# Optimization experiments

Hardware: AMD Instinct MI355X
Metric: run time of the kernel (lower is better)

The kernel has to match this reference:

```python
import jax, jax.numpy as jnp
import numpy as np

B, S, D, H, NUM_REL = 8, 1024, 1024, 16, 512
HD = D // H  # head size = 64


def setup_inputs() -> dict:
    key = jax.random.key(0)
    ks = jax.random.split(key, 12)
    sc = 0.02  # weight init scale for numerical stability
    inp = {
        "query": jax.random.normal(ks[0], (B, S, D), jnp.float32),
        "key": jax.random.normal(ks[1], (B, S, D), jnp.float32),
        "value": jax.random.normal(ks[2], (B, S, D), jnp.float32),
        "Wq": jax.random.normal(ks[3], (D, D), jnp.float32) * sc,
        "bq": jnp.zeros((D,), jnp.float32),
        "Wk": jax.random.normal(ks[4], (D, D), jnp.float32) * sc,
        "bk": jnp.zeros((D,), jnp.float32),
        "Wv": jax.random.normal(ks[5], (D, D), jnp.float32) * sc,
        "bv": jnp.zeros((D,), jnp.float32),
        "Wo": jax.random.normal(ks[6], (D, D), jnp.float32) * sc,
        "bo": jnp.zeros((D,), jnp.float32),
        "pos_table": jax.random.normal(ks[7], (NUM_REL, HD), jnp.float32) * sc,
        # True = masked position (causal: cannot attend to future)
        "mask": jnp.broadcast_to(jnp.triu(jnp.ones((S, S), bool), k=1), (B, S, S)),
    }
    return inp


def reference(query, key, value, Wq, bq, Wk, bk, Wv, bv, Wo, bo, pos_table, mask):
    Bq, Sq, Dm = query.shape
    hd = Dm // H

    def proj(x, W, b):
        # nn.Linear: x @ W.T + b, then split heads -> [B, H, S, hd]
        return (x @ W.T + b).reshape(Bq, Sq, H, hd).transpose(0, 2, 1, 3)

    q = proj(query, Wq, bq)
    k = proj(key, Wk, bk)
    v = proj(value, Wv, bv)

    scores = jnp.einsum("bhid,bhjd->bhij", q, k)

    # relative-position bias: idxs[i,j] = clip(i - j, 0, NUM_REL-1)
    t = jnp.arange(Sq)
    idxs = jnp.clip(t[:, None] - t[None, :], 0, pos_table.shape[0] - 1)
    pos = pos_table[idxs]  # [S, S, hd]
    scores = scores + jnp.einsum("bhid,ijd->bhij", q, pos)

    scores = scores / np.sqrt(hd).astype(np.float32)
    scores = jnp.where(mask[:, None, :, :], jnp.float32(-1e9), scores)
    prob = jax.nn.softmax(scores, axis=-1)  # dropout p=0.0 -> identity

    out = jnp.einsum("bhij,bhjd->bhid", prob, v)
    out = out.transpose(0, 2, 1, 3).reshape(Bq, Sq, Dm)
    return out @ Wo.T + bo
```

## Files before the change

### kernel.cpp

```cpp
#include <hip/hip_runtime.h>
#include <stdint.h>

#define DEV __device__ __forceinline__

typedef unsigned short u16;
typedef __bf16 bf16x8 __attribute__((ext_vector_type(8)));
typedef float  f32x4  __attribute__((ext_vector_type(4)));
typedef unsigned short u16x8 __attribute__((ext_vector_type(8)));
typedef unsigned short u16x4 __attribute__((ext_vector_type(4)));
typedef float  fvec4  __attribute__((ext_vector_type(4)));

constexpr int Sz   = 1024;
constexpr int Dm   = 1024;
constexpr int HDm  = 64;
constexpr int NREL = 512;
constexpr int Mrows = 8192;
constexpr int KV   = 32;

DEV u16 f2bf(float f) { return __builtin_bit_cast(u16, (__bf16)f); }
DEV float bf2f(u16 h) { return __builtin_bit_cast(float, (uint32_t)h << 16); }
DEV f32x4 mfma16(bf16x8 a, bf16x8 b, f32x4 c) {
  return __builtin_amdgcn_mfma_f32_16x16x32_bf16(a, b, c, 0, 0, 0);
}
DEV float ex2(float x) {
  float r;
  asm("v_exp_f32 %0, %1" : "=v"(r) : "v"(x));
  return r;
}

DEV u16x4 tr0(const u16* p) {
  u16x4 d;
  asm volatile("ds_read_b64_tr_b16 %0, %1"
               : "=v"(d)
               : "v"((const __attribute__((address_space(3))) u16*)p));
  return d;
}
DEV u16x4 tr512(const u16* p) {
  u16x4 d;
  asm volatile("ds_read_b64_tr_b16 %0, %1 offset:512"
               : "=v"(d)
               : "v"((const __attribute__((address_space(3))) u16*)p));
  return d;
}
DEV bf16x8 mk8(u16x4 a, u16x4 b) {
  u16x8 r;
  r[0] = a[0]; r[1] = a[1]; r[2] = a[2]; r[3] = a[3];
  r[4] = b[0]; r[5] = b[1]; r[6] = b[2]; r[7] = b[3];
  return __builtin_bit_cast(bf16x8, r);
}
DEV void gload(const u16* src, u16* dst) {
  __builtin_amdgcn_global_load_lds(
      (const __attribute__((address_space(1))) void*)src,
      (__attribute__((address_space(3))) void*)dst, 16, 0, 0);
}

__global__ __launch_bounds__(256) void cvtw_kernel(const float* __restrict__ w0,
                                                   const float* __restrict__ w1,
                                                   const float* __restrict__ w2,
                                                   const float* __restrict__ w3,
                                                   const float* __restrict__ ps,
                                                   u16* __restrict__ o0,
                                                   u16* __restrict__ o1,
                                                   u16* __restrict__ o2,
                                                   u16* __restrict__ o3,
                                                   u16* __restrict__ op) {
  const int bid = blockIdx.x;
  const float* in;
  u16* out;
  int local;
  if (bid < 4096) {
    const int s = bid >> 10;
    in = s == 0 ? w0 : s == 1 ? w1 : s == 2 ? w2 : w3;
    out = s == 0 ? o0 : s == 1 ? o1 : s == 2 ? o2 : o3;
    local = bid & 1023;
  } else {
    in = ps; out = op; local = bid - 4096;
  }
  size_t i = (size_t)local * 256 + threadIdx.x;
  fvec4 v = *(const fvec4*)(in + i * 4);
  u16x4 o;
  o[0] = f2bf(v[0]); o[1] = f2bf(v[1]); o[2] = f2bf(v[2]); o[3] = f2bf(v[3]);
  *(u16x4*)(out + i * 4) = o;
}

template<bool OUT_BF16>
DEV void gemm_epilogue(const float* bias, void* Cout, int m0, int n0,
                       int wr, int wc, int lr, int lg, f32x4 acc[4][4]) {
  #pragma unroll
  for (int m = 0; m < 4; ++m) {
    const int grow = m0 + wr + m * 16 + lr;
    #pragma unroll
    for (int n = 0; n < 4; ++n) {
      const int gcol = n0 + wc + n * 16 + lg * 4;
      fvec4 bb = *(const fvec4*)&bias[gcol];
      if (OUT_BF16) {
        u16x4 w;
        #pragma unroll
        for (int r = 0; r < 4; ++r) w[r] = f2bf(acc[m][n][r] + bb[r]);
        *(u16x4*)&((u16*)Cout)[(size_t)grow * Dm + gcol] = w;
      } else {
        fvec4 w;
        #pragma unroll
        for (int r = 0; r < 4; ++r) w[r] = acc[m][n][r] + bb[r];
        *(fvec4*)&((float*)Cout)[(size_t)grow * Dm + gcol] = w;
      }
    }
  }
}

DEV void gemm_compute(const u16* Ab, const u16* Bb, int wr, int wc,
                      int lr, int lg, f32x4 acc[4][4]) {
  #pragma unroll
  for (int kk = 0; kk < 2; ++kk) {
    bf16x8 af[4], bf_[4];
    #pragma unroll
    for (int m = 0; m < 4; ++m)
      af[m] = *(const bf16x8*)&Ab[(wr + m * 16 + lr) * 64 + (((kk * 4 + lg) ^ (lr & 7)) * 8)];
    #pragma unroll
    for (int n = 0; n < 4; ++n)
      bf_[n] = *(const bf16x8*)&Bb[(wc + n * 16 + lr) * 64 + (((kk * 4 + lg) ^ (lr & 7)) * 8)];
    __builtin_amdgcn_s_setprio(1);
    #pragma unroll
    for (int m = 0; m < 4; ++m)
      #pragma unroll
      for (int n = 0; n < 4; ++n)
        acc[m][n] = mfma16(bf_[n], af[m], acc[m][n]);
    __builtin_amdgcn_s_setprio(0);
  }
}

template<bool OUT_BF16>
DEV void gemm_body16(const u16* __restrict__ A, const u16* __restrict__ Bw,
                     const float* __restrict__ bias, void* __restrict__ Cout,
                     int m0, int n0, u16* As, u16* Bs) {
  const int tid = threadIdx.x;
  const int wave = tid >> 6, lane = tid & 63;
  const int lr = lane & 15, lg = lane >> 4;
  const int wr = (wave >> 1) * 64, wc = (wave & 1) * 64;

  auto issue = [&](int t) {
    const int k0 = t * 64;
    u16* Ad = As + (t & 1) * (128 * 64);
    u16* Bd = Bs + (t & 1) * (128 * 64);
    #pragma unroll
    for (int it = 0; it < 4; ++it) {
      int chunk = it * 256 + tid;
      int row = chunk >> 3, c16 = chunk & 7;
      gload(Bw + (size_t)(n0 + row) * Dm + k0 + ((c16 ^ (row & 7)) * 8),
            Bd + (it * 256 + wave * 64) * 8);
      gload(A + (size_t)(m0 + row) * Dm + k0 + ((c16 ^ (row & 7)) * 8),
            Ad + (it * 256 + wave * 64) * 8);
    }
  };

  issue(0);
  f32x4 acc[4][4] = {};
  for (int t = 0; t < 16; ++t) {
    if (t < 15) {
      issue(t + 1);
      asm volatile("s_waitcnt vmcnt(8)" ::: "memory");
    } else {
      asm volatile("s_waitcnt vmcnt(0)" ::: "memory");
    }
    __builtin_amdgcn_s_barrier();
    gemm_compute(As + (t & 1) * (128 * 64), Bs + (t & 1) * (128 * 64),
                 wr, wc, lr, lg, acc);
    __builtin_amdgcn_s_barrier();
  }
  gemm_epilogue<OUT_BF16>(bias, Cout, m0, n0, wr, wc, lr, lg, acc);
}

template<bool OUT_BF16>
DEV void gemm_body32(const float* __restrict__ A, const u16* __restrict__ Bw,
                     const float* __restrict__ bias, void* __restrict__ Cout,
                     int m0, int n0, u16* As, u16* Bs) {
  const int tid = threadIdx.x;
  const int wave = tid >> 6, lane = tid & 63;
  const int lr = lane & 15, lg = lane >> 4;
  const int wr = (wave >> 1) * 64, wc = (wave & 1) * 64;

  fvec4 ar[4][2];
  auto loadA = [&](int t) {
    const int k0 = t * 64;
    #pragma unroll
    for (int it = 0; it < 4; ++it) {
      int chunk = it * 256 + tid;
      int rw = chunk >> 3, cc = chunk & 7;
      const float* src = A + (size_t)(m0 + rw) * Dm + k0 + cc * 8;
      ar[it][0] = *(const fvec4*)src;
      ar[it][1] = *(const fvec4*)(src + 4);
    }
  };
  auto issueB = [&](int t) {
    const int k0 = t * 64;
    u16* Bd = Bs + (t & 1) * (128 * 64);
    #pragma unroll
    for (int it = 0; it < 4; ++it) {
      int chunk = it * 256 + tid;
      int rw = chunk >> 3, cc = chunk & 7;
      gload(Bw + (size_t)(n0 + rw) * Dm + k0 + ((cc ^ (rw & 7)) * 8),
            Bd + (it * 256 + wave * 64) * 8);
    }
  };

  loadA(0);
  __builtin_amdgcn_sched_barrier(0);
  issueB(0);
  __builtin_amdgcn_sched_barrier(0);

  f32x4 acc[4][4] = {};
  for (int t = 0; t < 16; ++t) {
    asm volatile("s_waitcnt vmcnt(4)" ::: "memory");
    __builtin_amdgcn_sched_barrier(0);
    u16* Ad = As + (t & 1) * (128 * 64);
    #pragma unroll
    for (int it = 0; it < 4; ++it) {
      int chunk = it * 256 + tid;
      int rw = chunk >> 3, cc = chunk & 7;
      u16x8 v;
      #pragma unroll
      for (int e = 0; e < 4; ++e) { v[e] = f2bf(ar[it][0][e]); v[e + 4] = f2bf(ar[it][1][e]); }
      *(u16x8*)&Ad[rw * 64 + ((cc ^ (rw & 7)) * 8)] = v;
    }
    __builtin_amdgcn_sched_barrier(0);
    if (t < 15) {
      loadA(t + 1);
      __builtin_amdgcn_sched_barrier(0);
      issueB(t + 1);
      __builtin_amdgcn_sched_barrier(0);
      asm volatile("s_waitcnt vmcnt(12)" ::: "memory");
    } else {
      asm volatile("s_waitcnt vmcnt(0)" ::: "memory");
    }
    asm volatile("s_waitcnt lgkmcnt(0)" ::: "memory");
    __builtin_amdgcn_s_barrier();
    gemm_compute(Ad, Bs + (t & 1) * (128 * 64), wr, wc, lr, lg, acc);
    __builtin_amdgcn_s_barrier();
  }
  gemm_epilogue<OUT_BF16>(bias, Cout, m0, n0, wr, wc, lr, lg, acc);
}

template<bool OUT_BF16>
__global__ __launch_bounds__(256) void gemm1_kernel(const u16* __restrict__ A,
                                                    const u16* __restrict__ Bw,
                                                    const float* __restrict__ bias,
                                                    void* __restrict__ Cout) {
  __shared__ u16 As[2 * 128 * 64];
  __shared__ u16 Bs[2 * 128 * 64];
  const int r = blockIdx.x;
  const int xcd = r & 7, loc = r >> 3;
  const int m0 = (xcd * 8 + (loc & 7)) * 128;
  const int n0 = (loc >> 3) * 128;
  gemm_body16<OUT_BF16>(A, Bw, bias, Cout, m0, n0, As, Bs);
}

__global__ __launch_bounds__(256) void gemm3_kernel(
    const float* __restrict__ Xq, const float* __restrict__ Xk, const float* __restrict__ Xv,
    const u16* __restrict__ Wq, const u16* __restrict__ Wk, const u16* __restrict__ Wv,
    const float* __restrict__ bq, const float* __restrict__ bk, const float* __restrict__ bv,
    u16* __restrict__ Cq, u16* __restrict__ Ck, u16* __restrict__ Cv) {
  __shared__ u16 As[2 * 128 * 64];
  __shared__ u16 Bs[2 * 128 * 64];
  const int flat = blockIdx.x;
  const int seg = flat >> 9;
  const int r = flat & 511;
  const int xcd = r & 7, loc = r >> 3;
  const int m0 = (xcd * 8 + (loc & 7)) * 128;
  const int n0 = (loc >> 3) * 128;
  const float* A = seg == 0 ? Xq : seg == 1 ? Xk : Xv;
  const u16* Bw = seg == 0 ? Wq : seg == 1 ? Wk : Wv;
  const float* bias = seg == 0 ? bq : seg == 1 ? bk : bv;
  u16* C = seg == 0 ? Cq : seg == 1 ? Ck : Cv;
  gemm_body32<true>(A, Bw, bias, C, m0, n0, As, Bs);
}

__global__ __launch_bounds__(256, 4) void attn_kernel(const u16* __restrict__ Q,
                                                      const u16* __restrict__ Kb,
                                                      const u16* __restrict__ Vb,
                                                      const u16* __restrict__ posB,
                                                      u16* __restrict__ O) {
  __shared__ u16 Ks[2][KV * 64];
  __shared__ u16 Vs[2][KV * 64];
  __shared__ u16 ring[128 * 64];
  __shared__ u16 SH[4][16 * 40];

  const int tid = threadIdx.x;
  const int wave = tid >> 6, lane = tid & 63;
  const int lr = lane & 15, lg = lane >> 4;
  const int bid = blockIdx.x;
  const int xcd = bid & 7;
  const int idx = bid >> 3;
  const int bhl = idx & 15;
  const int pp_ = idx >> 4;
  const int bh  = xcd * 16 + bhl;
  const int b = bh >> 4, h = bh & 15;

  u16* SHW = SH[wave];
  const size_t rowbase = (size_t)(b * Sz) * Dm + h * HDm;

  const int krow = tid >> 3, kc = tid & 7;
  const int vj = ((tid >> 5) << 2) | ((tid >> 1) & 3);
  const int vd = ((tid >> 3) & 3) * 16 + (tid & 1) * 8;
  const int rrow = tid >> 3, rcol = tid & 7;

  auto issueKV = [&](int t) {
    const int j0 = t * KV;
    const int bsel = t & 1;
    gload(Kb + rowbase + (size_t)(j0 + krow) * Dm + ((kc ^ (krow & 7)) * 8),
          &Ks[bsel][wave * 512]);
    gload(Vb + rowbase + (size_t)(j0 + vj) * Dm + vd, &Vs[bsel][wave * 512]);
  };
  auto stageRing = [&](int cb) {
    const int rel = cb + rrow;
    const int slot = rel & 127;
    const int cl = rel < 0 ? 0 : (rel > NREL - 1 ? NREL - 1 : rel);
    gload(posB + cl * 64 + ((rcol ^ (slot & 7)) * 8),
          &ring[((cb & 127) + wave * 8) * 64]);
  };

  constexpr float SC = 0.125f * 1.44269504f;

  for (int job = 0; job < 2; ++job) {
    const int qi = job ? pp_ : 15 - pp_;
    const int qb = qi * 64;
    const int wq = qb + wave * 16;
    const int nt = 2 * qi + 2;
    const int qg = wq + lr;

    const u16* qptr = Q + rowbase + (size_t)(wq + lr) * Dm;
    bf16x8 qf[2];
    qf[0] = *(const bf16x8*)(qptr + lg * 8);
    qf[1] = *(const bf16x8*)(qptr + 32 + lg * 8);

    float b511;
    {
      const u16* pp = posB + (NREL - 1) * HDm;
      bf16x8 pa0 = *(const bf16x8*)(pp + lg * 8);
      bf16x8 pa1 = *(const bf16x8*)(pp + 32 + lg * 8);
      f32x4 a = {};
      a = mfma16(pa0, qf[0], a);
      a = mfma16(pa1, qf[1], a);
      b511 = a[0];
    }

    stageRing(qb + 32);
    stageRing(qb);
    stageRing(qb - 32);
    issueKV(0);

    f32x4 oacc[4] = {};
    float m_i = -1e30f, l_i = 0.f;

    for (int t = 0; t < nt; ++t) {
      const int j0 = t * KV;
      const int bsel = t & 1;
      const bool active = (j0 <= wq + 15);
      const bool clamp = (wq - j0 - 31) >= NREL - 1;
      const int wb = wq - j0 - 31;

      if (t + 1 < nt) {
        stageRing(qb - 32 * (t + 1) - 32);
        issueKV(t + 1);
        asm volatile("s_waitcnt vmcnt(3)" ::: "memory");
      } else {
        asm volatile("s_waitcnt vmcnt(0)" ::: "memory");
      }
      __builtin_amdgcn_s_barrier();

      if (active) {
        if (!clamp) {
          #pragma unroll
          for (int wg = 0; wg < 3; ++wg) {
            const int rrel = wb + wg * 16 + lr;
            const int slot = rrel & 127;
            const u16* rp = &ring[slot * 64];
            f32x4 a = {};
            a = mfma16(qf[0], *(const bf16x8*)&rp[((0 + lg) ^ (slot & 7)) * 8], a);
            a = mfma16(qf[1], *(const bf16x8*)&rp[((4 + lg) ^ (slot & 7)) * 8], a);
            #pragma unroll
            for (int r = 0; r < 4; ++r) {
              const int q = lg * 4 + r;
              const int col = q - (wg * 16 + lr) + 31;
              if (col >= 0 && col < 32)
                SHW[q * 40 + col] = f2bf(a[r]);
            }
          }
        }

        __builtin_amdgcn_s_setprio(1);
        f32x4 s0 = {}, s1 = {};
        const u16* KT = &Ks[bsel][0];
        s0 = mfma16(*(const bf16x8*)&KT[(0 + lr) * 64 + (((0 + lg) ^ (lr & 7)) * 8)], qf[0], s0);
        s0 = mfma16(*(const bf16x8*)&KT[(0 + lr) * 64 + (((4 + lg) ^ (lr & 7)) * 8)], qf[1], s0);
        s1 = mfma16(*(const bf16x8*)&KT[(16 + lr) * 64 + (((0 + lg) ^ (lr & 7)) * 8)], qf[0], s1);
        s1 = mfma16(*(const bf16x8*)&KT[(16 + lr) * 64 + (((4 + lg) ^ (lr & 7)) * 8)], qf[1], s1);
        __builtin_amdgcn_s_setprio(0);

        float p0[4], p1[4];
        float tmax = -3e38f;
        if (clamp) {
          #pragma unroll
          for (int r = 0; r < 4; ++r) {
            p0[r] = (s0[r] + b511) * SC; tmax = fmaxf(tmax, p0[r]);
            p1[r] = (s1[r] + b511) * SC; tmax = fmaxf(tmax, p1[r]);
          }
        } else {
          u16x4 bv0 = *(const u16x4*)&SHW[lr * 40 + lg * 4];
          u16x4 bv1 = *(const u16x4*)&SHW[lr * 40 + 16 + lg * 4];
          #pragma unroll
          for (int r = 0; r < 4; ++r) {
            float v0 = (s0[r] + bf2f(bv0[r])) * SC;
            if (j0 + lg * 4 + r > qg) v0 = -1e9f;
            p0[r] = v0; tmax = fmaxf(tmax, v0);
            float v1 = (s1[r] + bf2f(bv1[r])) * SC;
            if (j0 + 16 + lg * 4 + r > qg) v1 = -1e9f;
            p1[r] = v1; tmax = fmaxf(tmax, v1);
          }
        }
        tmax = fmaxf(tmax, __shfl_xor(tmax, 16));
        tmax = fmaxf(tmax, __shfl_xor(tmax, 32));

        if (!__all(tmax <= m_i + 11.5f)) {
          float mn = fmaxf(m_i, tmax);
          float sc = ex2(m_i - mn);
          m_i = mn; l_i *= sc;
          #pragma unroll
          for (int dg = 0; dg < 4; ++dg) oacc[dg] *= sc;
        }

        float lsum = 0.f;
        #pragma unroll
        for (int r = 0; r < 4; ++r) {
          p0[r] = ex2(p0[r] - m_i); lsum += p0[r];
          p1[r] = ex2(p1[r] - m_i); lsum += p1[r];
        }
        lsum += __shfl_xor(lsum, 16);
        lsum += __shfl_xor(lsum, 32);
        l_i += lsum;

        u16x4 pk0, pk1;
        #pragma unroll
        for (int r = 0; r < 4; ++r) { pk0[r] = f2bf(p0[r]); pk1[r] = f2bf(p1[r]); }
        *(u16x4*)&SHW[lr * 40 + lg * 4] = pk0;
        *(u16x4*)&SHW[lr * 40 + 16 + lg * 4] = pk1;

        bf16x8 pB = *(const bf16x8*)&SHW[lr * 40 + lg * 8];

        u16x4 va[4][2];
        #pragma unroll
        for (int dg = 0; dg < 4; ++dg) {
          const u16* base = &Vs[bsel][(2 * lg) * 256 + dg * 64 + lr * 4];
          va[dg][0] = tr0(base);
          va[dg][1] = tr512(base);
        }
        asm volatile("s_waitcnt lgkmcnt(0)" ::: "memory");
        __builtin_amdgcn_sched_barrier(0);
        __builtin_amdgcn_s_setprio(1);
        #pragma unroll
        for (int dg = 0; dg < 4; ++dg)
          oacc[dg] = mfma16(mk8(va[dg][0], va[dg][1]), pB, oacc[dg]);
        __builtin_amdgcn_s_setprio(0);
      }
      __builtin_amdgcn_s_barrier();
    }

    const float inv = 1.0f / l_i;
    const size_t obase = rowbase + (size_t)qg * Dm;
    #pragma unroll
    for (int dg = 0; dg < 4; ++dg) {
      u16x4 w;
      #pragma unroll
      for (int r = 0; r < 4; ++r) w[r] = f2bf(oacc[dg][r] * inv);
      *(u16x4*)&O[obase + dg * 16 + lg * 4] = w;
    }
  }
}

extern "C" void kernel_launch(void* const* d_in, const int* in_sizes, int n_in,
                              void* d_out, int out_size, void* d_ws, size_t ws_size,
                              hipStream_t stream) {
  const float* query = (const float*)d_in[0];
  const float* key   = (const float*)d_in[1];
  const float* value = (const float*)d_in[2];
  const float* Wq    = (const float*)d_in[3];
  const float* bq    = (const float*)d_in[4];
  const float* Wk    = (const float*)d_in[5];
  const float* bk    = (const float*)d_in[6];
  const float* Wv    = (const float*)d_in[7];
  const float* bv    = (const float*)d_in[8];
  const float* Wo    = (const float*)d_in[9];
  const float* bo    = (const float*)d_in[10];
  const float* pos   = (const float*)d_in[11];

  char* ws = (char*)d_ws;
  u16* WqB  = (u16*)(ws);
  u16* WkB  = (u16*)(ws + (2ull << 20));
  u16* WvB  = (u16*)(ws + (4ull << 20));
  u16* WoB  = (u16*)(ws + (6ull << 20));
  u16* posB = (u16*)(ws + (8ull << 20));
  u16* Qb   = (u16*)(ws + (9ull << 20));
  u16* Kb   = (u16*)(ws + (25ull << 20));
  u16* Vb   = (u16*)(ws + (41ull << 20));
  u16* Ob   = (u16*)(ws + (57ull << 20));

  cvtw_kernel<<<4128, 256, 0, stream>>>(Wq, Wk, Wv, Wo, pos,
                                        WqB, WkB, WvB, WoB, posB);

  gemm3_kernel<<<1536, 256, 0, stream>>>(query, key, value, WqB, WkB, WvB,
                                         bq, bk, bv, Qb, Kb, Vb);

  attn_kernel<<<1024, 256, 0, stream>>>(Qb, Kb, Vb, posB, Ob);

  gemm1_kernel<false><<<512, 256, 0, stream>>>(Ob, WoB, bo, d_out);
}
```

Before: 183.4 us.

## Deepen QKV projection GEMM pipeline to prefetch two k-tiles ahead

The fp32-input QKV projection GEMM now keeps two register sets of A-tile data and a triple-buffered B tile in shared memory, so global loads are issued two iterations ahead instead of one. The A shared tile becomes single-buffered, since each step converts from registers just before compute and is guarded by barriers. The aim is to hide more global-memory latency for the large fp32 A reads. The cost is more registers for the second A buffer and different LDS use (one A buffer plus three B buffers), which may reduce occupancy.

```diff
diff --git a/kernel.cpp b/kernel.cpp
--- a/kernel.cpp
+++ b/kernel.cpp
@@ -109,7 +109,7 @@
 }
 
 DEV void gemm_compute(const u16* Ab, const u16* Bb, int wr, int wc,
-                      int lr, int lg, f32x4 acc[4][4]) {
+                      int lr, int lg, f32x4 (&acc)[4][4]) {
   #pragma unroll
   for (int kk = 0; kk < 2; ++kk) {
     bf16x8 af[4], bf_[4];
@@ -179,21 +179,20 @@
   const int lr = lane & 15, lg = lane >> 4;
   const int wr = (wave >> 1) * 64, wc = (wave & 1) * 64;
 
-  fvec4 ar[4][2];
-  auto loadA = [&](int t) {
+  auto loadA = [&](int t, fvec4 (&arr)[4][2]) {
     const int k0 = t * 64;
     #pragma unroll
     for (int it = 0; it < 4; ++it) {
       int chunk = it * 256 + tid;
       int rw = chunk >> 3, cc = chunk & 7;
       const float* src = A + (size_t)(m0 + rw) * Dm + k0 + cc * 8;
-      ar[it][0] = *(const fvec4*)src;
-      ar[it][1] = *(const fvec4*)(src + 4);
+      arr[it][0] = *(const fvec4*)src;
+      arr[it][1] = *(const fvec4*)(src + 4);
     }
   };
   auto issueB = [&](int t) {
     const int k0 = t * 64;
-    u16* Bd = Bs + (t & 1) * (128 * 64);
+    u16* Bd = Bs + (t % 3) * (128 * 64);
     #pragma unroll
     for (int it = 0; it < 4; ++it) {
       int chunk = it * 256 + tid;
@@ -202,40 +201,57 @@
             Bd + (it * 256 + wave * 64) * 8);
     }
   };
-
-  loadA(0);
-  __builtin_amdgcn_sched_barrier(0);
-  issueB(0);
-  __builtin_amdgcn_sched_barrier(0);
-
-  f32x4 acc[4][4] = {};
-  for (int t = 0; t < 16; ++t) {
-    asm volatile("s_waitcnt vmcnt(4)" ::: "memory");
-    __builtin_amdgcn_sched_barrier(0);
-    u16* Ad = As + (t & 1) * (128 * 64);
+  auto writeA = [&](fvec4 (&arr)[4][2]) {
     #pragma unroll
     for (int it = 0; it < 4; ++it) {
       int chunk = it * 256 + tid;
       int rw = chunk >> 3, cc = chunk & 7;
       u16x8 v;
       #pragma unroll
-      for (int e = 0; e < 4; ++e) { v[e] = f2bf(ar[it][0][e]); v[e + 4] = f2bf(ar[it][1][e]); }
-      *(u16x8*)&Ad[rw * 64 + ((cc ^ (rw & 7)) * 8)] = v;
+      for (int e = 0; e < 4; ++e) { v[e] = f2bf(arr[it][0][e]); v[e + 4] = f2bf(arr[it][1][e]); }
+      *(u16x8*)&As[rw * 64 + ((cc ^ (rw & 7)) * 8)] = v;
+    }
+  };
+
+  fvec4 ar0[4][2], ar1[4][2];
+  loadA(0, ar0);
+  __builtin_amdgcn_sched_barrier(0);
+  issueB(0);
+  __builtin_amdgcn_sched_barrier(0);
+  loadA(1, ar1);
+  __builtin_amdgcn_sched_barrier(0);
+  issueB(1);
+  __builtin_amdgcn_sched_barrier(0);
+
+  f32x4 acc[4][4] = {};
+  auto step = [&](int t, fvec4 (&arr)[4][2]) {
+    if (t < 15) {
+      asm volatile("s_waitcnt vmcnt(16)" ::: "memory");
+    } else {
+      asm volatile("s_waitcnt vmcnt(4)" ::: "memory");
     }
     __builtin_amdgcn_sched_barrier(0);
-    if (t < 15) {
-      loadA(t + 1);
+    writeA(arr);
+    __builtin_amdgcn_sched_barrier(0);
+    if (t < 14) {
+      loadA(t + 2, arr);
       __builtin_amdgcn_sched_barrier(0);
-      issueB(t + 1);
+      issueB(t + 2);
       __builtin_amdgcn_sched_barrier(0);
+      asm volatile("s_waitcnt vmcnt(24)" ::: "memory");
+    } else if (t == 14) {
       asm volatile("s_waitcnt vmcnt(12)" ::: "memory");
     } else {
       asm volatile("s_waitcnt vmcnt(0)" ::: "memory");
     }
     asm volatile("s_waitcnt lgkmcnt(0)" ::: "memory");
     __builtin_amdgcn_s_barrier();
-    gemm_compute(Ad, Bs + (t & 1) * (128 * 64), wr, wc, lr, lg, acc);
+    gemm_compute(As, Bs + (t % 3) * (128 * 64), wr, wc, lr, lg, acc);
     __builtin_amdgcn_s_barrier();
+  };
+  for (int t = 0; t < 16; t += 2) {
+    step(t, ar0);
+    step(t + 1, ar1);
   }
   gemm_epilogue<OUT_BF16>(bias, Cout, m0, n0, wr, wc, lr, lg, acc);
 }
@@ -259,8 +275,8 @@
     const u16* __restrict__ Wq, const u16* __restrict__ Wk, const u16* __restrict__ Wv,
     const float* __restrict__ bq, const float* __restrict__ bk, const float* __restrict__ bv,
     u16* __restrict__ Cq, u16* __restrict__ Ck, u16* __restrict__ Cv) {
-  __shared__ u16 As[2 * 128 * 64];
-  __shared__ u16 Bs[2 * 128 * 64];
+  __shared__ u16 As[128 * 64];
+  __shared__ u16 Bs[3 * 128 * 64];
   const int flat = blockIdx.x;
   const int seg = flat >> 9;
   const int r = flat & 511;
```

Result: no change. 179.8 us (-1.9%).
